# Kernel optimization log

Hardware: AMD Instinct MI355X
Metric: run time of the kernel (lower is better)

The kernel has to match this reference:

```python
import jax, jax.numpy as jnp
import numpy as np

B, T, D, N = 32, 512, 1024, 1024


def setup_inputs() -> dict:
    key = jax.random.key(0)
    k1, k2, k3, k4, k5 = jax.random.split(key, 5)
    x = jax.random.normal(k1, (B, T, D), dtype=jnp.float32)
    h0 = jnp.zeros((B, N), dtype=jnp.float32)  # self.h Variable init
    # GRUCell params: gate kernel [D+N, 2N], candidate kernel [D+N, N]
    Wg = jax.random.normal(k2, (D + N, 2 * N), dtype=jnp.float32) * 0.05
    bg = jax.random.normal(k3, (2 * N,), dtype=jnp.float32) * 0.05 + 1.0  # TF gate bias init 1.0
    Wc = jax.random.normal(k4, (D + N, N), dtype=jnp.float32) * 0.05
    bc = jax.random.normal(k5, (N,), dtype=jnp.float32) * 0.05
    return {"x": x, "h0": h0, "Wg": Wg, "bg": bg, "Wc": Wc, "bc": bc}


def reference(x, h0, Wg, bg, Wc, bc):
    # tf.nn.rnn_cell.GRUCell recurrence via dynamic_rnn, single layer
    def step(h, x_t):
        xh = jnp.concatenate([x_t, h], axis=-1)           # [B, D+N]
        gates = jax.nn.sigmoid(xh @ Wg + bg)              # [B, 2N]
        r, u = jnp.split(gates, 2, axis=-1)
        xrh = jnp.concatenate([x_t, r * h], axis=-1)      # [B, D+N]
        c = jnp.tanh(xrh @ Wc + bc)                       # [B, N]
        h_new = u * h + (1.0 - u) * c
        return h_new, h_new

    xs = jnp.swapaxes(x, 0, 1)                            # [T, B, D]
    _, outs = jax.lax.scan(step, h0, xs)                  # outs: [T, B, N]
    outputs = jnp.swapaxes(outs, 0, 1)                    # [B, T, N]
    activations = outputs.reshape(-1, N)                  # [B*T, N]
    return activations
```

## Files before the change

### kernel.cpp

```cpp
#include <hip/hip_runtime.h>
#include <hip/hip_bf16.h>

#define B_ 32
#define T_ 512
#define D_ 1024
#define N_ 1024
#define NWG 192
#define NGATE 128
#define TPB 256
#define SMEM_BYTES (131072 + 8192 + 64 + 2112)

typedef __attribute__((ext_vector_type(8))) short short8v;
typedef __attribute__((ext_vector_type(4))) float f32x4;

__device__ __forceinline__ float bf2f(unsigned short u) {
  union { float f; unsigned int i; } c; c.i = ((unsigned int)u) << 16; return c.f;
}
__device__ __forceinline__ unsigned short f2bf(float f) {
  union { float f; unsigned int i; } c; c.f = f;
  unsigned int r = c.i + 0x7FFFu + ((c.i >> 16) & 1u);
  return (unsigned short)(r >> 16);
}
__device__ __forceinline__ unsigned cvtpk(float a, float b) {
  unsigned r;
  asm("v_cvt_pk_bf16_f32 %0, %1, %2" : "=v"(r) : "v"(a), "v"(b));
  return r;
}
__device__ __forceinline__ short8v pack_frag(f32x4 lo, f32x4 hi) {
  union { unsigned u[4]; short8v s; } c;
  c.u[0] = cvtpk(lo[0], lo[1]); c.u[1] = cvtpk(lo[2], lo[3]);
  c.u[2] = cvtpk(hi[0], hi[1]); c.u[3] = cvtpk(hi[2], hi[3]);
  return c.s;
}

__device__ __forceinline__ void st_bf16_sc(unsigned short* p, unsigned short v) {
  asm volatile("global_store_short %0, %1, off sc0 sc1"
               :: "v"((unsigned long long)p), "v"((unsigned)v) : "memory");
}
__device__ __forceinline__ void st_f32_sc(float* p, float v) {
  asm volatile("global_store_dword %0, %1, off sc0 sc1"
               :: "v"((unsigned long long)p), "v"(v) : "memory");
}

__device__ __forceinline__ void flag_store(unsigned* line, unsigned v) {
  __hip_atomic_store(line, v, __ATOMIC_RELAXED, __HIP_MEMORY_SCOPE_AGENT);
}
__device__ __forceinline__ void poll64(unsigned* base, int lane, unsigned tgt) {
  unsigned* p = base + (size_t)lane * 16;
  int tries = 0;
  for (;;) {
    unsigned v = __hip_atomic_load(p, __ATOMIC_RELAXED, __HIP_MEMORY_SCOPE_AGENT);
    if (__all((int)(v >= tgt))) break;
    __builtin_amdgcn_s_sleep(1);
    if (++tries > (1 << 20)) break;
  }
}
__device__ __forceinline__ void poll128(unsigned* base, int lane, unsigned tgt) {
  unsigned* p0 = base + (size_t)lane * 16;
  unsigned* p1 = base + (size_t)(64 + lane) * 16;
  int tries = 0;
  for (;;) {
    unsigned v0 = __hip_atomic_load(p0, __ATOMIC_RELAXED, __HIP_MEMORY_SCOPE_AGENT);
    unsigned v1 = __hip_atomic_load(p1, __ATOMIC_RELAXED, __HIP_MEMORY_SCOPE_AGENT);
    if (__all((int)(v0 >= tgt && v1 >= tgt))) break;
    __builtin_amdgcn_s_sleep(1);
    if (++tries > (1 << 20)) break;
  }
}

__device__ __forceinline__ int frag_off(int m, int k) {
  const int mt = m >> 4, ks = k >> 5, kk = k & 31;
  const int l = (m & 15) + (((kk >> 2) & 3) << 4);
  const int j = (kk & 3) + ((kk >> 4) << 2);
  return ((mt * 32 + ks) * 64 + l) * 8 + j;
}

template <int KS>
__device__ __forceinline__ void build_xfrags(const float* __restrict__ x, int t,
                                             int kbase, int lane,
                                             short8v frag[2][KS]) {
#pragma unroll
  for (int mt = 0; mt < 2; ++mt) {
    const int m = mt * 16 + (lane & 15);
    const float* row = x + ((size_t)m * T_ + t) * D_;
#pragma unroll
    for (int ks = 0; ks < KS; ++ks) {
      const int k0 = kbase + ks * 32 + ((lane >> 4) << 2);
      f32x4 lo = *(const f32x4*)(row + k0);
      f32x4 hi = *(const f32x4*)(row + k0 + 16);
      frag[mt][ks] = pack_frag(lo, hi);
    }
  }
}

template <int KS>
__device__ __forceinline__ void mfma_reg(const short8v frag[2][KS],
                                         const unsigned short* __restrict__ ldsW,
                                         int ksg0, f32x4* acc, int lane) {
#pragma unroll
  for (int mt = 0; mt < 2; ++mt)
#pragma unroll
    for (int ks = 0; ks < KS; ++ks) {
      const int ksg = ksg0 + ks;
      short8v bhi = *(const short8v*)(ldsW + ((size_t)(0 * 64 + ksg) * 64 + lane) * 8);
      short8v blo = *(const short8v*)(ldsW + ((size_t)(1 * 64 + ksg) * 64 + lane) * 8);
      acc[mt] = __builtin_amdgcn_mfma_f32_16x16x32_bf16(frag[mt][ks], bhi, acc[mt], 0, 0, 0);
      acc[mt] = __builtin_amdgcn_mfma_f32_16x16x32_bf16(frag[mt][ks], blo, acc[mt], 0, 0, 0);
    }
}

__device__ __forceinline__ void gate_hphase(
    const unsigned short* __restrict__ hq, int ks0,
    const unsigned short* __restrict__ ldsW, int ksg0,
    f32x4* acc, int lane, bool loadh, const float* __restrict__ hsrc, f32x4& hvec)
{
  short8v areg[2][16];
  if (loadh)
    asm volatile("global_load_dwordx4 %0, %1, off sc0 sc1"
                 : "=v"(hvec) : "v"((unsigned long long)hsrc) : "memory");
#pragma unroll
  for (int mt = 0; mt < 2; ++mt)
#pragma unroll
    for (int ks = 0; ks < 16; ++ks) {
      const unsigned short* p = hq + ((size_t)((mt * 32 + ks0 + ks) * 64 + lane)) * 8;
      asm volatile("global_load_dwordx4 %0, %1, off sc0 sc1"
                   : "=v"(areg[mt][ks]) : "v"((unsigned long long)p) : "memory");
    }
  asm volatile("s_waitcnt vmcnt(0)" ::: "memory");
  __builtin_amdgcn_sched_barrier(0);
#pragma unroll
  for (int mt = 0; mt < 2; ++mt)
#pragma unroll
    for (int ks = 0; ks < 16; ++ks) {
      const int ksg = ksg0 + ks;
      short8v bhi = *(const short8v*)(ldsW + ((size_t)(0 * 64 + ksg) * 64 + lane) * 8);
      short8v blo = *(const short8v*)(ldsW + ((size_t)(1 * 64 + ksg) * 64 + lane) * 8);
      acc[mt] = __builtin_amdgcn_mfma_f32_16x16x32_bf16(areg[mt][ks], bhi, acc[mt], 0, 0, 0);
      acc[mt] = __builtin_amdgcn_mfma_f32_16x16x32_bf16(areg[mt][ks], blo, acc[mt], 0, 0, 0);
    }
}

__device__ __forceinline__ void cand_bphase(
    const unsigned short* __restrict__ rhq, int ks0,
    const unsigned short* __restrict__ ldsW, int ksg0,
    f32x4* acc, int lane,
    const float* up0, const float* up1, float& uv0, float& uv1)
{
  short8v areg[2][8];
  asm volatile("global_load_dword %0, %2, off sc0 sc1\n\t"
               "global_load_dword %1, %3, off sc0 sc1"
               : "=&v"(uv0), "=&v"(uv1)
               : "v"((unsigned long long)up0), "v"((unsigned long long)up1)
               : "memory");
#pragma unroll
  for (int mt = 0; mt < 2; ++mt)
#pragma unroll
    for (int ks = 0; ks < 8; ++ks) {
      const unsigned short* p = rhq + ((size_t)((mt * 32 + ks0 + ks) * 64 + lane)) * 8;
      asm volatile("global_load_dwordx4 %0, %1, off sc0 sc1"
                   : "=v"(areg[mt][ks]) : "v"((unsigned long long)p) : "memory");
    }
  asm volatile("s_waitcnt vmcnt(0)" ::: "memory");
  __builtin_amdgcn_sched_barrier(0);
#pragma unroll
  for (int mt = 0; mt < 2; ++mt)
#pragma unroll
    for (int ks = 0; ks < 8; ++ks) {
      const int ksg = ksg0 + ks;
      short8v bhi = *(const short8v*)(ldsW + ((size_t)(0 * 64 + ksg) * 64 + lane) * 8);
      short8v blo = *(const short8v*)(ldsW + ((size_t)(1 * 64 + ksg) * 64 + lane) * 8);
      acc[mt] = __builtin_amdgcn_mfma_f32_16x16x32_bf16(areg[mt][ks], bhi, acc[mt], 0, 0, 0);
      acc[mt] = __builtin_amdgcn_mfma_f32_16x16x32_bf16(areg[mt][ks], blo, acc[mt], 0, 0, 0);
    }
}

__global__ __launch_bounds__(TPB, 1) void gru_persistent(
    const float* __restrict__ x, const float* __restrict__ h0,
    const float* __restrict__ Wg, const float* __restrict__ bg,
    const float* __restrict__ Wc, const float* __restrict__ bc,
    float* __restrict__ out,
    unsigned* __restrict__ ctrs,
    unsigned short* __restrict__ hq,
    unsigned short* __restrict__ rhq,
    float* __restrict__ u_buf,
    float* __restrict__ h_buf)
{
  const int wg = blockIdx.x;
  const int tid = threadIdx.x;
  const int lane = tid & 63;
  const int wv = tid >> 6;

  extern __shared__ char smem[];
  unsigned short* ldsW = (unsigned short*)smem;
  float* ldsR = (float*)(smem + 131072);
  float* ldsBias = (float*)(smem + 131072 + 8192);
  float* ldsH = (float*)(smem + 131072 + 8192 + 64);

  unsigned* flagH = ctrs;
  unsigned* flagG = ctrs + 64 * 16;

  const bool is_gate = wg < NGATE;
  const int c0 = (is_gate ? wg : (wg - NGATE)) * 16;
  const float* Wsrc = is_gate ? Wg : Wc;
  const int ldw = is_gate ? 2 * N_ : N_;
  const float* bias = is_gate ? bg : bc;

  const int col = tid & 15, row = tid >> 4;
  const int colg = c0 + col;
  const int b0 = row, b1 = 16 + row;

  for (int i = tid; i < 64 * 64; i += TPB) {
    const int ks = i >> 6, l = i & 63;
    const int n = l & 15, kqp = (l >> 4) * 4;
#pragma unroll
    for (int j = 0; j < 8; ++j) {
      const int k = ks * 32 + ((j < 4) ? 0 : 16) + kqp + (j & 3);
      const float w = Wsrc[(size_t)k * ldw + c0 + n];
      const unsigned short hi = f2bf(w);
      const unsigned short lo = f2bf(w - bf2f(hi));
      ldsW[((size_t)(0 * 64 + ks) * 64 + l) * 8 + j] = hi;
      ldsW[((size_t)(1 * 64 + ks) * 64 + l) * 8 + j] = lo;
    }
  }
  if (tid < 16) ldsBias[tid] = bias[c0 + tid];
  __syncthreads();

  if (is_gate) {
    const bool r_wg = (c0 < N_);
    unsigned* myflag = flagG + (size_t)wg * 16;
    for (int t = 0; t < T_; ++t) {
      f32x4 acc[2] = {{0.f,0.f,0.f,0.f},{0.f,0.f,0.f,0.f}};
      f32x4 hvec = {0.f,0.f,0.f,0.f};
      if (wv < 2) {
        short8v xf[2][16];
        build_xfrags<16>(x, t, wv * 512, lane, xf);
        mfma_reg<16>(xf, ldsW, wv * 16, acc, lane);
      } else {
        poll64(flagH, lane, (unsigned)(t + 1));
        const int idx = tid - 128;
        const float* hsrc = h_buf + (size_t)(c0 + (idx & 15)) * 32 + (idx >> 4) * 4;
        gate_hphase(hq, (wv - 2) * 16, ldsW, 32 + (wv - 2) * 16, acc, lane,
                    r_wg, hsrc, hvec);
        if (r_wg) {
          float* d = ldsH + (idx & 15) * 33 + (idx >> 4) * 4;
          d[0] = hvec[0]; d[1] = hvec[1]; d[2] = hvec[2]; d[3] = hvec[3];
        }
      }
#pragma unroll
      for (int mt = 0; mt < 2; ++mt)
#pragma unroll
        for (int r = 0; r < 4; ++r)
          ldsR[(wv * 2 + mt) * 256 + (4 * (lane >> 4) + r) * 16 + (lane & 15)] = acc[mt][r];
      __syncthreads();
      {
        float s0 = ldsR[0 * 256 + tid] + ldsR[2 * 256 + tid]
                 + ldsR[4 * 256 + tid] + ldsR[6 * 256 + tid];
        float s1 = ldsR[1 * 256 + tid] + ldsR[3 * 256 + tid]
                 + ldsR[5 * 256 + tid] + ldsR[7 * 256 + tid];
        float p0 = fminf(fmaxf(s0 + ldsBias[col], -30.f), 30.f);
        float p1 = fminf(fmaxf(s1 + ldsBias[col], -30.f), 30.f);
        const float g0 = 1.f / (1.f + __expf(-p0));
        const float g1 = 1.f / (1.f + __expf(-p1));
        if (r_wg) {
          const float hv0 = ldsH[col * 33 + row];
          const float hv1 = ldsH[col * 33 + row + 16];
          st_bf16_sc(rhq + frag_off(b0, colg), f2bf(g0 * hv0));
          st_bf16_sc(rhq + frag_off(b1, colg), f2bf(g1 * hv1));
        } else {
          st_f32_sc(u_buf + b0 * N_ + (colg - N_), g0);
          st_f32_sc(u_buf + b1 * N_ + (colg - N_), g1);
        }
      }
      asm volatile("s_waitcnt vmcnt(0)" ::: "memory");
      __syncthreads();
      if (tid == 0) flag_store(myflag, (unsigned)(t + 1));
    }
  } else {
    unsigned* myflag = flagH + (size_t)(wg - NGATE) * 16;
    float hreg0 = h0[b0 * N_ + colg];
    float hreg1 = h0[b1 * N_ + colg];
    st_f32_sc(h_buf + (size_t)colg * 32 + b0, hreg0);
    st_f32_sc(h_buf + (size_t)colg * 32 + b1, hreg1);
    st_bf16_sc(hq + frag_off(b0, colg), f2bf(hreg0));
    st_bf16_sc(hq + frag_off(b1, colg), f2bf(hreg1));
    asm volatile("s_waitcnt vmcnt(0)" ::: "memory");
    __syncthreads();
    if (tid == 0) flag_store(myflag, 1u);

    f32x4 acc[2] = {{0.f,0.f,0.f,0.f},{0.f,0.f,0.f,0.f}};
    {
      short8v xf[2][8];
      build_xfrags<8>(x, 0, wv * 256, lane, xf);
      mfma_reg<8>(xf, ldsW, wv * 8, acc, lane);
    }
    for (int t = 0; t < T_; ++t) {
      poll128(flagG, lane, (unsigned)(t + 1));
      float uv0, uv1;
      cand_bphase(rhq, wv * 8, ldsW, 32 + wv * 8, acc, lane,
                  u_buf + b0 * N_ + colg, u_buf + b1 * N_ + colg, uv0, uv1);
#pragma unroll
      for (int mt = 0; mt < 2; ++mt)
#pragma unroll
        for (int r = 0; r < 4; ++r)
          ldsR[(wv * 2 + mt) * 256 + (4 * (lane >> 4) + r) * 16 + (lane & 15)] = acc[mt][r];
      __syncthreads();
      {
        float s0 = ldsR[0 * 256 + tid] + ldsR[2 * 256 + tid]
                 + ldsR[4 * 256 + tid] + ldsR[6 * 256 + tid];
        float s1 = ldsR[1 * 256 + tid] + ldsR[3 * 256 + tid]
                 + ldsR[5 * 256 + tid] + ldsR[7 * 256 + tid];
        float p0 = fminf(fmaxf(s0 + ldsBias[col], -20.f), 20.f);
        float p1 = fminf(fmaxf(s1 + ldsBias[col], -20.f), 20.f);
        const float e0 = __expf(2.f * p0), e1 = __expf(2.f * p1);
        const float c0v = (e0 - 1.f) / (e0 + 1.f);
        const float c1v = (e1 - 1.f) / (e1 + 1.f);
        const float hn0 = uv0 * hreg0 + (1.f - uv0) * c0v;
        const float hn1 = uv1 * hreg1 + (1.f - uv1) * c1v;
        hreg0 = hn0; hreg1 = hn1;
        st_bf16_sc(hq + frag_off(b0, colg), f2bf(hn0));
        st_bf16_sc(hq + frag_off(b1, colg), f2bf(hn1));
        st_f32_sc(h_buf + (size_t)colg * 32 + b0, hn0);
        st_f32_sc(h_buf + (size_t)colg * 32 + b1, hn1);
        out[((size_t)b0 * T_ + t) * N_ + colg] = hn0;
        out[((size_t)b1 * T_ + t) * N_ + colg] = hn1;
      }
      asm volatile("s_waitcnt vmcnt(0)" ::: "memory");
      __syncthreads();
      if (tid == 0) flag_store(myflag, (unsigned)(t + 2));
      if (t + 1 < T_) {
        acc[0] = (f32x4){0.f,0.f,0.f,0.f};
        acc[1] = (f32x4){0.f,0.f,0.f,0.f};
        short8v xf[2][8];
        build_xfrags<8>(x, t + 1, wv * 256, lane, xf);
        mfma_reg<8>(xf, ldsW, wv * 8, acc, lane);
      }
    }
  }
}

extern "C" void kernel_launch(void* const* d_in, const int* in_sizes, int n_in,
                              void* d_out, int out_size, void* d_ws, size_t ws_size,
                              hipStream_t stream) {
  const float* x  = (const float*)d_in[0];
  const float* h0 = (const float*)d_in[1];
  const float* Wg = (const float*)d_in[2];
  const float* bg = (const float*)d_in[3];
  const float* Wc = (const float*)d_in[4];
  const float* bc = (const float*)d_in[5];
  float* out = (float*)d_out;

  char* w = (char*)d_ws;
  unsigned* ctrs       = (unsigned*)(w + 0);
  unsigned short* hq   = (unsigned short*)(w + 16384);
  unsigned short* rhq  = (unsigned short*)(w + 81920);
  float* u_buf         = (float*)(w + 147456);
  float* h_buf         = (float*)(w + 278528);

  hipFuncSetAttribute((const void*)gru_persistent,
                      hipFuncAttributeMaxDynamicSharedMemorySize, SMEM_BYTES);
  hipMemsetAsync(w, 0, 16384, stream);
  gru_persistent<<<NWG, TPB, SMEM_BYTES, stream>>>(
      x, h0, Wg, bg, Wc, bc, out, ctrs, hq, rhq, u_buf, h_buf);
}
```

Before: 3.664 ms.

## Narrow flag polling to true dependencies and precompute gate x-projection off critical path

Gate workgroups now split the x and h halves of the matmul across all four waves, computing the x-projection for step t+1 right after publishing step t, so only the h half sits on the critical path. Flag polling is narrowed from all producer flags to the specific producers each wave depends on: the h-column slice it reads plus the matching column for r. Candidate workgroups wait only on the r-gate flags first, and check the u-gate flags after their matmul. The aim is to cut cross-workgroup synchronization latency and serial work per timestep, at the cost of more complex dependency reasoning and a risk of ordering errors.

```diff
diff --git a/kernel.cpp b/kernel.cpp
--- a/kernel.cpp
+++ b/kernel.cpp
@@ -45,24 +45,12 @@
 __device__ __forceinline__ void flag_store(unsigned* line, unsigned v) {
   __hip_atomic_store(line, v, __ATOMIC_RELAXED, __HIP_MEMORY_SCOPE_AGENT);
 }
-__device__ __forceinline__ void poll64(unsigned* base, int lane, unsigned tgt) {
-  unsigned* p = base + (size_t)lane * 16;
+__device__ __forceinline__ void poll_pred(const unsigned* p, bool act, unsigned tgt) {
   int tries = 0;
   for (;;) {
-    unsigned v = __hip_atomic_load(p, __ATOMIC_RELAXED, __HIP_MEMORY_SCOPE_AGENT);
+    unsigned v = tgt;
+    if (act) v = __hip_atomic_load(p, __ATOMIC_RELAXED, __HIP_MEMORY_SCOPE_AGENT);
     if (__all((int)(v >= tgt))) break;
-    __builtin_amdgcn_s_sleep(1);
-    if (++tries > (1 << 20)) break;
-  }
-}
-__device__ __forceinline__ void poll128(unsigned* base, int lane, unsigned tgt) {
-  unsigned* p0 = base + (size_t)lane * 16;
-  unsigned* p1 = base + (size_t)(64 + lane) * 16;
-  int tries = 0;
-  for (;;) {
-    unsigned v0 = __hip_atomic_load(p0, __ATOMIC_RELAXED, __HIP_MEMORY_SCOPE_AGENT);
-    unsigned v1 = __hip_atomic_load(p1, __ATOMIC_RELAXED, __HIP_MEMORY_SCOPE_AGENT);
-    if (__all((int)(v0 >= tgt && v1 >= tgt))) break;
     __builtin_amdgcn_s_sleep(1);
     if (++tries > (1 << 20)) break;
   }
@@ -106,71 +94,6 @@
       short8v blo = *(const short8v*)(ldsW + ((size_t)(1 * 64 + ksg) * 64 + lane) * 8);
       acc[mt] = __builtin_amdgcn_mfma_f32_16x16x32_bf16(frag[mt][ks], bhi, acc[mt], 0, 0, 0);
       acc[mt] = __builtin_amdgcn_mfma_f32_16x16x32_bf16(frag[mt][ks], blo, acc[mt], 0, 0, 0);
-    }
-}
-
-__device__ __forceinline__ void gate_hphase(
-    const unsigned short* __restrict__ hq, int ks0,
-    const unsigned short* __restrict__ ldsW, int ksg0,
-    f32x4* acc, int lane, bool loadh, const float* __restrict__ hsrc, f32x4& hvec)
-{
-  short8v areg[2][16];
-  if (loadh)
-    asm volatile("global_load_dwordx4 %0, %1, off sc0 sc1"
-                 : "=v"(hvec) : "v"((unsigned long long)hsrc) : "memory");
-#pragma unroll
-  for (int mt = 0; mt < 2; ++mt)
-#pragma unroll
-    for (int ks = 0; ks < 16; ++ks) {
-      const unsigned short* p = hq + ((size_t)((mt * 32 + ks0 + ks) * 64 + lane)) * 8;
-      asm volatile("global_load_dwordx4 %0, %1, off sc0 sc1"
-                   : "=v"(areg[mt][ks]) : "v"((unsigned long long)p) : "memory");
-    }
-  asm volatile("s_waitcnt vmcnt(0)" ::: "memory");
-  __builtin_amdgcn_sched_barrier(0);
-#pragma unroll
-  for (int mt = 0; mt < 2; ++mt)
-#pragma unroll
-    for (int ks = 0; ks < 16; ++ks) {
-      const int ksg = ksg0 + ks;
-      short8v bhi = *(const short8v*)(ldsW + ((size_t)(0 * 64 + ksg) * 64 + lane) * 8);
-      short8v blo = *(const short8v*)(ldsW + ((size_t)(1 * 64 + ksg) * 64 + lane) * 8);
-      acc[mt] = __builtin_amdgcn_mfma_f32_16x16x32_bf16(areg[mt][ks], bhi, acc[mt], 0, 0, 0);
-      acc[mt] = __builtin_amdgcn_mfma_f32_16x16x32_bf16(areg[mt][ks], blo, acc[mt], 0, 0, 0);
-    }
-}
-
-__device__ __forceinline__ void cand_bphase(
-    const unsigned short* __restrict__ rhq, int ks0,
-    const unsigned short* __restrict__ ldsW, int ksg0,
-    f32x4* acc, int lane,
-    const float* up0, const float* up1, float& uv0, float& uv1)
-{
-  short8v areg[2][8];
-  asm volatile("global_load_dword %0, %2, off sc0 sc1\n\t"
-               "global_load_dword %1, %3, off sc0 sc1"
-               : "=&v"(uv0), "=&v"(uv1)
-               : "v"((unsigned long long)up0), "v"((unsigned long long)up1)
-               : "memory");
-#pragma unroll
-  for (int mt = 0; mt < 2; ++mt)
-#pragma unroll
-    for (int ks = 0; ks < 8; ++ks) {
-      const unsigned short* p = rhq + ((size_t)((mt * 32 + ks0 + ks) * 64 + lane)) * 8;
-      asm volatile("global_load_dwordx4 %0, %1, off sc0 sc1"
-                   : "=v"(areg[mt][ks]) : "v"((unsigned long long)p) : "memory");
-    }
-  asm volatile("s_waitcnt vmcnt(0)" ::: "memory");
-  __builtin_amdgcn_sched_barrier(0);
-#pragma unroll
-  for (int mt = 0; mt < 2; ++mt)
-#pragma unroll
-    for (int ks = 0; ks < 8; ++ks) {
-      const int ksg = ksg0 + ks;
-      short8v bhi = *(const short8v*)(ldsW + ((size_t)(0 * 64 + ksg) * 64 + lane) * 8);
-      short8v blo = *(const short8v*)(ldsW + ((size_t)(1 * 64 + ksg) * 64 + lane) * 8);
-      acc[mt] = __builtin_amdgcn_mfma_f32_16x16x32_bf16(areg[mt][ks], bhi, acc[mt], 0, 0, 0);
-      acc[mt] = __builtin_amdgcn_mfma_f32_16x16x32_bf16(areg[mt][ks], blo, acc[mt], 0, 0, 0);
     }
 }
 
@@ -228,29 +151,56 @@
   if (is_gate) {
     const bool r_wg = (c0 < N_);
     unsigned* myflag = flagG + (size_t)wg * 16;
+    const unsigned* pollp = nullptr; bool pact = false;
+    if (lane < 16)                { pollp = flagH + (size_t)(16 * wv + lane) * 16; pact = true; }
+    else if (lane == 16 && r_wg)  { pollp = flagH + (size_t)wg * 16;               pact = true; }
+
+    f32x4 accA[2] = {{0.f,0.f,0.f,0.f},{0.f,0.f,0.f,0.f}};
+    {
+      short8v xf[2][8];
+      build_xfrags<8>(x, 0, wv * 256, lane, xf);
+      mfma_reg<8>(xf, ldsW, wv * 8, accA, lane);
+    }
     for (int t = 0; t < T_; ++t) {
-      f32x4 acc[2] = {{0.f,0.f,0.f,0.f},{0.f,0.f,0.f,0.f}};
+      poll_pred(pollp, pact, (unsigned)(t + 1));
       f32x4 hvec = {0.f,0.f,0.f,0.f};
-      if (wv < 2) {
-        short8v xf[2][16];
-        build_xfrags<16>(x, t, wv * 512, lane, xf);
-        mfma_reg<16>(xf, ldsW, wv * 16, acc, lane);
-      } else {
-        poll64(flagH, lane, (unsigned)(t + 1));
-        const int idx = tid - 128;
-        const float* hsrc = h_buf + (size_t)(c0 + (idx & 15)) * 32 + (idx >> 4) * 4;
-        gate_hphase(hq, (wv - 2) * 16, ldsW, 32 + (wv - 2) * 16, acc, lane,
-                    r_wg, hsrc, hvec);
-        if (r_wg) {
-          float* d = ldsH + (idx & 15) * 33 + (idx >> 4) * 4;
-          d[0] = hvec[0]; d[1] = hvec[1]; d[2] = hvec[2]; d[3] = hvec[3];
-        }
-      }
+      const bool do_h = r_wg && (tid < 128);
+      if (do_h) {
+        const float* hsrc = h_buf + (size_t)(c0 + (tid & 15)) * 32 + (tid >> 4) * 4;
+        asm volatile("global_load_dwordx4 %0, %1, off sc0 sc1"
+                     : "=v"(hvec) : "v"((unsigned long long)hsrc) : "memory");
+      }
+      short8v areg[2][8];
+#pragma unroll
+      for (int mt = 0; mt < 2; ++mt)
+#pragma unroll
+        for (int ks = 0; ks < 8; ++ks) {
+          const unsigned short* p =
+              hq + ((size_t)((mt * 32 + wv * 8 + ks) * 64 + lane)) * 8;
+          asm volatile("global_load_dwordx4 %0, %1, off sc0 sc1"
+                       : "=v"(areg[mt][ks]) : "v"((unsigned long long)p) : "memory");
+        }
+      asm volatile("s_waitcnt vmcnt(0)" ::: "memory");
+      __builtin_amdgcn_sched_barrier(0);
+      if (do_h) {
+        float* d = ldsH + (tid & 15) * 33 + (tid >> 4) * 4;
+        d[0] = hvec[0]; d[1] = hvec[1]; d[2] = hvec[2]; d[3] = hvec[3];
+      }
+#pragma unroll
+      for (int mt = 0; mt < 2; ++mt)
+#pragma unroll
+        for (int ks = 0; ks < 8; ++ks) {
+          const int ksg = 32 + wv * 8 + ks;
+          short8v bhi = *(const short8v*)(ldsW + ((size_t)(0 * 64 + ksg) * 64 + lane) * 8);
+          short8v blo = *(const short8v*)(ldsW + ((size_t)(1 * 64 + ksg) * 64 + lane) * 8);
+          accA[mt] = __builtin_amdgcn_mfma_f32_16x16x32_bf16(areg[mt][ks], bhi, accA[mt], 0, 0, 0);
+          accA[mt] = __builtin_amdgcn_mfma_f32_16x16x32_bf16(areg[mt][ks], blo, accA[mt], 0, 0, 0);
+        }
 #pragma unroll
       for (int mt = 0; mt < 2; ++mt)
 #pragma unroll
         for (int r = 0; r < 4; ++r)
-          ldsR[(wv * 2 + mt) * 256 + (4 * (lane >> 4) + r) * 16 + (lane & 15)] = acc[mt][r];
+          ldsR[(wv * 2 + mt) * 256 + (4 * (lane >> 4) + r) * 16 + (lane & 15)] = accA[mt][r];
       __syncthreads();
       {
         float s0 = ldsR[0 * 256 + tid] + ldsR[2 * 256 + tid]
@@ -274,9 +224,23 @@
       asm volatile("s_waitcnt vmcnt(0)" ::: "memory");
       __syncthreads();
       if (tid == 0) flag_store(myflag, (unsigned)(t + 1));
+      if (t + 1 < T_) {
+        accA[0] = (f32x4){0.f,0.f,0.f,0.f};
+        accA[1] = (f32x4){0.f,0.f,0.f,0.f};
+        short8v xf[2][8];
+        build_xfrags<8>(x, t + 1, wv * 256, lane, xf);
+        mfma_reg<8>(xf, ldsW, wv * 8, accA, lane);
+      }
     }
   } else {
-    unsigned* myflag = flagH + (size_t)(wg - NGATE) * 16;
+    const int cidx = wg - NGATE;
+    unsigned* myflag = flagH + (size_t)cidx * 16;
+    const unsigned* p1 = nullptr; bool a1 = false;
+    if (lane < 16)       { p1 = flagG + (size_t)(16 * wv + lane) * 16;  a1 = true; }
+    else if (lane == 16) { p1 = flagG + (size_t)(64 + cidx) * 16;       a1 = true; }
+    const unsigned* p2 = nullptr; bool a2 = false;
+    if (lane < 16)       { p2 = flagG + (size_t)(64 + 16 * wv + lane) * 16; a2 = true; }
+
     float hreg0 = h0[b0 * N_ + colg];
     float hreg1 = h0[b1 * N_ + colg];
     st_f32_sc(h_buf + (size_t)colg * 32 + b0, hreg0);
@@ -287,22 +251,49 @@
     __syncthreads();
     if (tid == 0) flag_store(myflag, 1u);
 
-    f32x4 acc[2] = {{0.f,0.f,0.f,0.f},{0.f,0.f,0.f,0.f}};
+    f32x4 accA[2] = {{0.f,0.f,0.f,0.f},{0.f,0.f,0.f,0.f}};
     {
       short8v xf[2][8];
       build_xfrags<8>(x, 0, wv * 256, lane, xf);
-      mfma_reg<8>(xf, ldsW, wv * 8, acc, lane);
+      mfma_reg<8>(xf, ldsW, wv * 8, accA, lane);
     }
     for (int t = 0; t < T_; ++t) {
-      poll128(flagG, lane, (unsigned)(t + 1));
+      poll_pred(p1, a1, (unsigned)(t + 1));
       float uv0, uv1;
-      cand_bphase(rhq, wv * 8, ldsW, 32 + wv * 8, acc, lane,
-                  u_buf + b0 * N_ + colg, u_buf + b1 * N_ + colg, uv0, uv1);
+      asm volatile("global_load_dword %0, %2, off sc0 sc1\n\t"
+                   "global_load_dword %1, %3, off sc0 sc1"
+                   : "=&v"(uv0), "=&v"(uv1)
+                   : "v"((unsigned long long)(u_buf + b0 * N_ + colg)),
+                     "v"((unsigned long long)(u_buf + b1 * N_ + colg))
+                   : "memory");
+      short8v areg[2][8];
+#pragma unroll
+      for (int mt = 0; mt < 2; ++mt)
+#pragma unroll
+        for (int ks = 0; ks < 8; ++ks) {
+          const unsigned short* p =
+              rhq + ((size_t)((mt * 32 + wv * 8 + ks) * 64 + lane)) * 8;
+          asm volatile("global_load_dwordx4 %0, %1, off sc0 sc1"
+                       : "=v"(areg[mt][ks]) : "v"((unsigned long long)p) : "memory");
+        }
+      asm volatile("s_waitcnt vmcnt(0)" ::: "memory");
+      __builtin_amdgcn_sched_barrier(0);
+#pragma unroll
+      for (int mt = 0; mt < 2; ++mt)
+#pragma unroll
+        for (int ks = 0; ks < 8; ++ks) {
+          const int ksg = 32 + wv * 8 + ks;
+          short8v bhi = *(const short8v*)(ldsW + ((size_t)(0 * 64 + ksg) * 64 + lane) * 8);
+          short8v blo = *(const short8v*)(ldsW + ((size_t)(1 * 64 + ksg) * 64 + lane) * 8);
+          accA[mt] = __builtin_amdgcn_mfma_f32_16x16x32_bf16(areg[mt][ks], bhi, accA[mt], 0, 0, 0);
+          accA[mt] = __builtin_amdgcn_mfma_f32_16x16x32_bf16(areg[mt][ks], blo, accA[mt], 0, 0, 0);
+        }
+      poll_pred(p2, a2, (unsigned)(t + 1));
 #pragma unroll
       for (int mt = 0; mt < 2; ++mt)
 #pragma unroll
         for (int r = 0; r < 4; ++r)
-          ldsR[(wv * 2 + mt) * 256 + (4 * (lane >> 4) + r) * 16 + (lane & 15)] = acc[mt][r];
+          ldsR[(wv * 2 + mt) * 256 + (4 * (lane >> 4) + r) * 16 + (lane & 15)] = accA[mt][r];
       __syncthreads();
       {
         float s0 = ldsR[0 * 256 + tid] + ldsR[2 * 256 + tid]
@@ -310,8 +301,8 @@
         float s1 = ldsR[1 * 256 + tid] + ldsR[3 * 256 + tid]
                  + ldsR[5 * 256 + tid] + ldsR[7 * 256 + tid];
         float p0 = fminf(fmaxf(s0 + ldsBias[col], -20.f), 20.f);
-        float p1 = fminf(fmaxf(s1 + ldsBias[col], -20.f), 20.f);
-        const float e0 = __expf(2.f * p0), e1 = __expf(2.f * p1);
+        float p1v = fminf(fmaxf(s1 + ldsBias[col], -20.f), 20.f);
+        const float e0 = __expf(2.f * p0), e1 = __expf(2.f * p1v);
         const float c0v = (e0 - 1.f) / (e0 + 1.f);
         const float c1v = (e1 - 1.f) / (e1 + 1.f);
         const float hn0 = uv0 * hreg0 + (1.f - uv0) * c0v;
@@ -328,11 +319,11 @@
       __syncthreads();
       if (tid == 0) flag_store(myflag, (unsigned)(t + 2));
       if (t + 1 < T_) {
-        acc[0] = (f32x4){0.f,0.f,0.f,0.f};
-        acc[1] = (f32x4){0.f,0.f,0.f,0.f};
+        accA[0] = (f32x4){0.f,0.f,0.f,0.f};
+        accA[1] = (f32x4){0.f,0.f,0.f,0.f};
         short8v xf[2][8];
         build_xfrags<8>(x, t + 1, wv * 256, lane, xf);
-        mfma_reg<8>(xf, ldsW, wv * 8, acc, lane);
+        mfma_reg<8>(xf, ldsW, wv * 8, accA, lane);
       }
     }
   }
```

Result: faster. 3.244 ms (-11.5%).
